# Performance work log

Measured on AMD Instinct MI355X. Metric: run time of the kernel, lower is better.

## Reference

```python
import jax, jax.numpy as jnp
import numpy as np

B, T, V, E, DH, H, M, W = 64, 50, 32000, 64, 128, 8, 256, 50


def setup_inputs() -> dict:
    key = jax.random.key(0)
    ks = jax.random.split(key, 18)
    sc = 0.02
    return {
        "x": jax.random.randint(ks[0], (B, T), 0, V),
        "tok_emb": jax.random.normal(ks[1], (V, E)) * sc,
        "pos_emb": jax.random.normal(ks[2], (W, E)) * sc,
        "Wq": jax.random.normal(ks[3], (H, E, DH)) * sc,
        "bq": jnp.zeros((H, DH)),
        "Wk": jax.random.normal(ks[4], (H, E, DH)) * sc,
        "bk": jnp.zeros((H, DH)),
        "Wv": jax.random.normal(ks[5], (H, E, DH)) * sc,
        "bv": jnp.zeros((H, DH)),
        "Wo": jax.random.normal(ks[6], (H * DH, E)) * sc,
        "bo": jnp.zeros((E,)),
        "W1": jax.random.normal(ks[7], (E, M)) * sc,
        "b1": jnp.zeros((M,)),
        "W2": jax.random.normal(ks[8], (M, E)) * sc,
        "b2": jnp.zeros((E,)),
        "Wf": jax.random.normal(ks[9], (E, V)) * sc,
        "bf": jnp.zeros((V,)),
    }


def reference(x, tok_emb, pos_emb, Wq, bq, Wk, bk, Wv, bv, Wo, bo, W1, b1, W2, b2, Wf, bf):
    b, t = x.shape
    h = tok_emb[x] + pos_emb[:t]  # [B,T,E]
    # batched per-head QKV projections (original loops over 8 heads)
    Q = jnp.einsum("bte,hed->bhtd", h, Wq) + bq[None, :, None, :]
    K = jnp.einsum("bte,hed->bhtd", h, Wk) + bk[None, :, None, :]
    Vv = jnp.einsum("bte,hed->bhtd", h, Wv) + bv[None, :, None, :]
    scores = jnp.einsum("bhtd,bhsd->bhts", Q, K) / (DH ** 0.5)
    # faithful to original: masked_fill(tril(scores) == 0, -inf)
    scores = jnp.where(jnp.tril(scores) == 0, -jnp.inf, scores)
    attn = jax.nn.softmax(scores, axis=-1)
    o = jnp.einsum("bhts,bhsd->bhtd", attn, Vv)
    o = o.transpose(0, 2, 1, 3).reshape(b, t, H * DH)  # concat heads
    a = o @ Wo + bo
    # NOTE: no residual connections in the original module
    m = jax.nn.gelu(a @ W1 + b1, approximate=False)
    y = m @ W2 + b2
    logits = y @ Wf + bf  # [B,T,V]
    return logits
```

## Files before the change

kernel.cpp:

```cpp
#include <hip/hip_runtime.h>
#include <math.h>

#define T_ 50
#define R_ 3200

using u16 = unsigned short;
typedef __attribute__((ext_vector_type(8))) __bf16 bf16x8;
typedef __attribute__((ext_vector_type(4))) float f32x4;

__device__ __forceinline__ float bf2f(u16 u) {
  union { unsigned int i; float f; } x; x.i = ((unsigned int)u) << 16; return x.f;
}
__device__ __forceinline__ u16 f2bf(float f) {
  union { float f; unsigned int i; } x; x.f = f;
  unsigned int r = x.i + 0x7FFFu + ((x.i >> 16) & 1u);
  return (u16)(r >> 16);
}
__device__ __forceinline__ void split2(float v, u16& hi, u16& lo) {
  hi = f2bf(v);
  lo = f2bf(v - bf2f(hi));
}
__device__ __forceinline__ float gelu_f(float v) {
  return 0.5f * v * (1.0f + erff(v * 0.70710678118654752f));
}

__global__ __launch_bounds__(256) void k_prep(
    const int* __restrict__ x, const float* __restrict__ tok, const float* __restrict__ pos,
    const float* __restrict__ Wq, const float* __restrict__ Wk, const float* __restrict__ Wv,
    const float* __restrict__ bq, const float* __restrict__ bk, const float* __restrict__ bv,
    const float* __restrict__ Wo, const float* __restrict__ W1, const float* __restrict__ W2,
    const float* __restrict__ Wf,
    u16* __restrict__ hH, u16* __restrict__ hL,
    u16* __restrict__ WqkvTh, u16* __restrict__ WqkvTl, float* __restrict__ bqkv,
    u16* __restrict__ WoTh, u16* __restrict__ WoTl,
    u16* __restrict__ W1Th, u16* __restrict__ W1Tl,
    u16* __restrict__ W2Th, u16* __restrict__ W2Tl,
    u16* __restrict__ WfTh, u16* __restrict__ WfTl) {
  __shared__ __align__(16) float tile[64][68];
  int bid = blockIdx.x;
  if (bid < 800) {
    int i = bid * 256 + threadIdx.x;
    int row = i >> 6, e = i & 63;
    int t = row % T_;
    int v = x[row];
    split2(tok[(long)v * 64 + e] + pos[t * 64 + e], hH[i], hL[i]);
    return;
  }
  if (bid < 1964) {
    int i = (bid - 800) * 256 + threadIdx.x;
    const int S0 = 196608, S1 = 3072, S2 = 65536, S3 = 16384;
    if (i < S0) {
      int n = i >> 6, e = i & 63;
      int p = n >> 10, rem = n & 1023;
      int hh_ = rem >> 7, d = rem & 127;
      const float* W = (p == 0) ? Wq : ((p == 1) ? Wk : Wv);
      split2(W[hh_ * 8192 + e * 128 + d], WqkvTh[i], WqkvTl[i]);
      return;
    }
    i -= S0;
    if (i < S1) { int p = i >> 10, rem = i & 1023;
      const float* bb = (p == 0) ? bq : ((p == 1) ? bk : bv);
      bqkv[i] = bb[rem]; return; }
    i -= S1;
    if (i < S2) { int n = i >> 10, k = i & 1023;
      split2(Wo[k * 64 + n], WoTh[i], WoTl[i]); return; }
    i -= S2;
    if (i < S3) { int n = i >> 6, k = i & 63;
      split2(W1[k * 256 + n], W1Th[i], W1Tl[i]); return; }
    i -= S3;
    { int n = i >> 8, k = i & 255;
      split2(W2[k * 64 + n], W2Th[i], W2Tl[i]); }
    return;
  }
  int n0 = (bid - 1964) * 64;
  for (int c = threadIdx.x; c < 1024; c += 256) {
    int k = c >> 4, ch = (c & 15) * 4;
    *(float4*)&tile[k][ch] = *(const float4*)&Wf[(long)k * 32000 + n0 + ch];
  }
  __syncthreads();
  for (int c = threadIdx.x; c < 1024; c += 256) {
    int n = c >> 4, ch = (c & 15) * 4;
    u16 th[4], tl[4];
#pragma unroll
    for (int j = 0; j < 4; ++j) split2(tile[ch + j][n], th[j], tl[j]);
    *(ushort4*)&WfTh[(long)(n0 + n) * 64 + ch] = *(ushort4*)th;
    *(ushort4*)&WfTl[(long)(n0 + n) * 64 + ch] = *(ushort4*)tl;
  }
}

__global__ __launch_bounds__(256) void k_attn(const float* __restrict__ QKV,
                                              u16* __restrict__ Oh,
                                              u16* __restrict__ Ol) {
  int bh = blockIdx.x;
  int b = bh >> 3, hd = bh & 7;
  __shared__ __align__(16) float Kl[64][133];
  __shared__ __align__(16) float Vl[T_][128];
  __shared__ float Qw[4][128];
  __shared__ float Pw[4][64];
  const int tid = threadIdx.x, lane = tid & 63, wave = tid >> 6;
  const float* base = QKV + (long)b * T_ * 3072 + hd * 128;
  for (int c = tid; c < T_ * 32; c += 256) {
    int s = c >> 5, c4 = (c & 31) * 4;
    float4 kv = *(const float4*)&base[(long)s * 3072 + 1024 + c4];
    Kl[s][c4] = kv.x; Kl[s][c4 + 1] = kv.y; Kl[s][c4 + 2] = kv.z; Kl[s][c4 + 3] = kv.w;
    *(float4*)&Vl[s][c4] = *(const float4*)&base[(long)s * 3072 + 2048 + c4];
  }
  for (int c = tid; c < 14 * 32; c += 256) {
    int s = 50 + (c >> 5), c4 = (c & 31) * 4;
    Kl[s][c4] = 0.f; Kl[s][c4 + 1] = 0.f; Kl[s][c4 + 2] = 0.f; Kl[s][c4 + 3] = 0.f;
  }
  __syncthreads();
  const float scale = 0.0883883476483184406f;
  for (int r = wave; r < T_; r += 4) {
    Qw[wave][lane] = base[(long)r * 3072 + lane];
    Qw[wave][64 + lane] = base[(long)r * 3072 + 64 + lane];
    float p = 0.f;
#pragma unroll 8
    for (int d = 0; d < 128; ++d) p += Qw[wave][d] * Kl[lane][d];
    float sc = (lane <= r) ? p * scale : -INFINITY;
    float mx = sc;
    mx = fmaxf(mx, __shfl_xor(mx, 32)); mx = fmaxf(mx, __shfl_xor(mx, 16));
    mx = fmaxf(mx, __shfl_xor(mx, 8));  mx = fmaxf(mx, __shfl_xor(mx, 4));
    mx = fmaxf(mx, __shfl_xor(mx, 2));  mx = fmaxf(mx, __shfl_xor(mx, 1));
    float e = expf(sc - mx);
    float sum = e;
    sum += __shfl_xor(sum, 32); sum += __shfl_xor(sum, 16); sum += __shfl_xor(sum, 8);
    sum += __shfl_xor(sum, 4);  sum += __shfl_xor(sum, 2);  sum += __shfl_xor(sum, 1);
    Pw[wave][lane] = e / sum;
    float o0 = 0.f, o1 = 0.f;
#pragma unroll 4
    for (int s = 0; s <= r; ++s) {
      float pv = Pw[wave][s];
      o0 += pv * Vl[s][lane];
      o1 += pv * Vl[s][64 + lane];
    }
    long orow = ((long)b * T_ + r) * 1024 + hd * 128;
    u16 hi, lo;
    split2(o0, hi, lo); Oh[orow + lane] = hi;      Ol[orow + lane] = lo;
    split2(o1, hi, lo); Oh[orow + 64 + lane] = hi; Ol[orow + 64 + lane] = lo;
  }
}

template <int BN, int BK, int ACT, int OSPLIT>
__global__ __launch_bounds__(256) void k_gemm(
    const u16* __restrict__ Ah, const u16* __restrict__ Al,
    const u16* __restrict__ Bth, const u16* __restrict__ Btl,
    const float* __restrict__ bias,
    float* __restrict__ C, u16* __restrict__ Ch, u16* __restrict__ Cl,
    int ldc, int K) {
  constexpr int BM = 64;
  constexpr int TN = BN / 16;
  constexpr int BKW = BK / 8;
  __shared__ __align__(16) u16 Bh[BN][BK + 8];
  __shared__ __align__(16) u16 Bl[BN][BK + 8];
  const int m0 = blockIdx.x * BM, n0 = blockIdx.y * BN;
  const int tid = threadIdx.x, lane = tid & 63, wave = tid >> 6;
  const int ln = lane & 15, quad = lane >> 4;
  const long arow = (long)(m0 + wave * 16 + ln) * K;
  f32x4 acc[TN];
#pragma unroll
  for (int tn = 0; tn < TN; ++tn)
#pragma unroll
    for (int i = 0; i < 4; ++i) acc[tn][i] = 0.f;

  for (int kk = 0; kk < K; kk += BK) {
#pragma unroll
    for (int c0 = 0; c0 < BN * BKW; c0 += 256) {
      int c = c0 + tid;
      int r = c / BKW, c8 = (c % BKW) * 8;
      *(uint4*)&Bh[r][c8] = *(const uint4*)&Bth[(long)(n0 + r) * K + kk + c8];
      *(uint4*)&Bl[r][c8] = *(const uint4*)&Btl[(long)(n0 + r) * K + kk + c8];
    }
    __syncthreads();
#pragma unroll
    for (int ks = 0; ks < BK / 32; ++ks) {
      bf16x8 a_h = *(const bf16x8*)&Ah[arow + kk + ks * 32 + quad * 8];
      bf16x8 a_l = *(const bf16x8*)&Al[arow + kk + ks * 32 + quad * 8];
#pragma unroll
      for (int tn = 0; tn < TN; ++tn) {
        bf16x8 b_h = *(const bf16x8*)&Bh[tn * 16 + ln][ks * 32 + quad * 8];
        bf16x8 b_l = *(const bf16x8*)&Bl[tn * 16 + ln][ks * 32 + quad * 8];
        acc[tn] = __builtin_amdgcn_mfma_f32_16x16x32_bf16(a_h, b_h, acc[tn], 0, 0, 0);
        acc[tn] = __builtin_amdgcn_mfma_f32_16x16x32_bf16(a_l, b_h, acc[tn], 0, 0, 0);
        acc[tn] = __builtin_amdgcn_mfma_f32_16x16x32_bf16(a_h, b_l, acc[tn], 0, 0, 0);
      }
    }
    __syncthreads();
  }
#pragma unroll
  for (int tn = 0; tn < TN; ++tn) {
    int col = n0 + tn * 16 + ln;
    float bv = bias[col];
#pragma unroll
    for (int rr = 0; rr < 4; ++rr) {
      float v = acc[tn][rr] + bv;
      if (ACT) v = gelu_f(v);
      long idx = (long)(m0 + wave * 16 + quad * 4 + rr) * ldc + col;
      if constexpr (OSPLIT) {
        u16 hi, lo; split2(v, hi, lo);
        Ch[idx] = hi; Cl[idx] = lo;
      } else {
        C[idx] = v;
      }
    }
  }
}

extern "C" void kernel_launch(void* const* d_in, const int* in_sizes, int n_in,
                              void* d_out, int out_size, void* d_ws, size_t ws_size,
                              hipStream_t stream) {
  const int*   x   = (const int*)d_in[0];
  const float* tok = (const float*)d_in[1];
  const float* pos = (const float*)d_in[2];
  const float* Wq  = (const float*)d_in[3];
  const float* bq  = (const float*)d_in[4];
  const float* Wk  = (const float*)d_in[5];
  const float* bk  = (const float*)d_in[6];
  const float* Wv  = (const float*)d_in[7];
  const float* bv  = (const float*)d_in[8];
  const float* Wo  = (const float*)d_in[9];
  const float* bo  = (const float*)d_in[10];
  const float* W1  = (const float*)d_in[11];
  const float* b1  = (const float*)d_in[12];
  const float* W2  = (const float*)d_in[13];
  const float* b2  = (const float*)d_in[14];
  const float* Wf  = (const float*)d_in[15];
  const float* bfv = (const float*)d_in[16];

  char* ws = (char*)d_ws;
  u16*   hH     = (u16*)(ws + 0);
  u16*   hL     = (u16*)(ws + 409600);
  float* QKV    = (float*)(ws + 819200);
  u16*   oH     = (u16*)(ws + 40140800);
  u16*   oL     = (u16*)(ws + 46694400);
  u16*   aH     = (u16*)(ws + 53248000);
  u16*   aL     = (u16*)(ws + 53657600);
  u16*   mH     = (u16*)(ws + 54067200);
  u16*   mL     = (u16*)(ws + 55705600);
  u16*   yH     = (u16*)(ws + 57344000);
  u16*   yL     = (u16*)(ws + 57753600);
  u16*   WqkvTh = (u16*)(ws + 58163200);
  u16*   WqkvTl = (u16*)(ws + 58556416);
  float* bqkv   = (float*)(ws + 58949632);
  u16*   WoTh   = (u16*)(ws + 58961920);
  u16*   WoTl   = (u16*)(ws + 59092992);
  u16*   W1Th   = (u16*)(ws + 59224064);
  u16*   W1Tl   = (u16*)(ws + 59256832);
  u16*   W2Th   = (u16*)(ws + 59289600);
  u16*   W2Tl   = (u16*)(ws + 59322368);
  u16*   WfTh   = (u16*)(ws + 59355136);
  u16*   WfTl   = (u16*)(ws + 63451136);
  float* out    = (float*)d_out;

  k_prep<<<dim3(2464), 256, 0, stream>>>(x, tok, pos, Wq, Wk, Wv, bq, bk, bv,
      Wo, W1, W2, Wf, hH, hL, WqkvTh, WqkvTl, bqkv, WoTh, WoTl,
      W1Th, W1Tl, W2Th, W2Tl, WfTh, WfTl);
  k_gemm<128, 64, 0, 0><<<dim3(50, 24), 256, 0, stream>>>(
      hH, hL, WqkvTh, WqkvTl, bqkv, QKV, nullptr, nullptr, 3072, 64);
  k_attn<<<dim3(512), 256, 0, stream>>>(QKV, oH, oL);
  k_gemm<64, 256, 0, 1><<<dim3(50, 1), 256, 0, stream>>>(
      oH, oL, WoTh, WoTl, bo, nullptr, aH, aL, 64, 1024);
  k_gemm<128, 64, 1, 1><<<dim3(50, 2), 256, 0, stream>>>(
      aH, aL, W1Th, W1Tl, b1, nullptr, mH, mL, 256, 64);
  k_gemm<64, 256, 0, 1><<<dim3(50, 1), 256, 0, stream>>>(
      mH, mL, W2Th, W2Tl, b2, nullptr, yH, yL, 64, 256);
  k_gemm<128, 64, 0, 0><<<dim3(50, 250), 256, 0, stream>>>(
      yH, yL, WfTh, WfTl, bfv, out, nullptr, nullptr, 32000, 64);
}
```

Baseline: 602.8 us.

## Fuse MLP chain, restructure attention, drop LDS staging in GEMM, add XCD swizzle

Merges the output-projection, W1+GELU and W2 GEMMs into one k_mlp kernel that keeps intermediates in shared memory, removing two launches and global round-trips. The attention kernel now processes four query rows per wave, with XOR-swizzled K and transposed V in LDS and vectorized loads. The generic GEMM reads B fragments straight from global memory instead of staging them in LDS, swaps the MFMA operands so the epilogue can write float4/ushort4 rows, and optionally remaps block IDs across XCDs for the large logits GEMM. The costs are more redundant global reads of B and a small 200-block MLP kernel with one wave per block, which may leave much of the device idle.

```diff
diff --git a/kernel.cpp b/kernel.cpp
--- a/kernel.cpp
+++ b/kernel.cpp
@@ -91,118 +91,262 @@
 __global__ __launch_bounds__(256) void k_attn(const float* __restrict__ QKV,
                                               u16* __restrict__ Oh,
                                               u16* __restrict__ Ol) {
-  int bh = blockIdx.x;
-  int b = bh >> 3, hd = bh & 7;
-  __shared__ __align__(16) float Kl[64][133];
-  __shared__ __align__(16) float Vl[T_][128];
-  __shared__ float Qw[4][128];
-  __shared__ float Pw[4][64];
+  __shared__ __align__(16) float Kl[64 * 128];
+  __shared__ __align__(16) float Vt[128 * 64];
+  __shared__ __align__(16) float Qw[4][512];
+  __shared__ __align__(16) float Pw[4][256];
+  const int bh = blockIdx.x, b = bh >> 3, hd = bh & 7;
   const int tid = threadIdx.x, lane = tid & 63, wave = tid >> 6;
   const float* base = QKV + (long)b * T_ * 3072 + hd * 128;
-  for (int c = tid; c < T_ * 32; c += 256) {
-    int s = c >> 5, c4 = (c & 31) * 4;
-    float4 kv = *(const float4*)&base[(long)s * 3072 + 1024 + c4];
-    Kl[s][c4] = kv.x; Kl[s][c4 + 1] = kv.y; Kl[s][c4 + 2] = kv.z; Kl[s][c4 + 3] = kv.w;
-    *(float4*)&Vl[s][c4] = *(const float4*)&base[(long)s * 3072 + 2048 + c4];
-  }
-  for (int c = tid; c < 14 * 32; c += 256) {
-    int s = 50 + (c >> 5), c4 = (c & 31) * 4;
-    Kl[s][c4] = 0.f; Kl[s][c4 + 1] = 0.f; Kl[s][c4 + 2] = 0.f; Kl[s][c4 + 3] = 0.f;
+  for (int c = tid; c < 64 * 32; c += 256) {
+    int s = c >> 5, c4 = c & 31;
+    float4 kv = make_float4(0.f, 0.f, 0.f, 0.f), vv = kv;
+    if (s < T_) {
+      const float* rowp = base + (long)s * 3072;
+      kv = *(const float4*)(rowp + 1024 + c4 * 4);
+      vv = *(const float4*)(rowp + 2048 + c4 * 4);
+    }
+    *(float4*)&Kl[s * 128 + ((c4 ^ (s & 31)) << 2)] = kv;
+    int d0 = c4 * 4, s4 = s >> 2, sm = s & 3;
+    Vt[(d0 + 0) * 64 + ((s4 ^ ((d0 + 0) & 15)) << 2) + sm] = vv.x;
+    Vt[(d0 + 1) * 64 + ((s4 ^ ((d0 + 1) & 15)) << 2) + sm] = vv.y;
+    Vt[(d0 + 2) * 64 + ((s4 ^ ((d0 + 2) & 15)) << 2) + sm] = vv.z;
+    Vt[(d0 + 3) * 64 + ((s4 ^ ((d0 + 3) & 15)) << 2) + sm] = vv.w;
   }
   __syncthreads();
   const float scale = 0.0883883476483184406f;
-  for (int r = wave; r < T_; r += 4) {
-    Qw[wave][lane] = base[(long)r * 3072 + lane];
-    Qw[wave][64 + lane] = base[(long)r * 3072 + 64 + lane];
-    float p = 0.f;
+  for (int g = wave; g < 13; g += 4) {
+    const int r0 = g * 4;
+#pragma unroll
+    for (int it = 0; it < 2; ++it) {
+      int cc = lane + it * 64;
+      int j = cc >> 5, c4q = cc & 31;
+      int rq = r0 + j;
+      if (rq < T_)
+        *(float4*)&Qw[wave][j * 128 + c4q * 4] =
+            *(const float4*)&base[(long)rq * 3072 + c4q * 4];
+    }
+    asm volatile("s_waitcnt lgkmcnt(0)" ::: "memory");
+    float p0 = 0.f, p1 = 0.f, p2 = 0.f, p3 = 0.f;
 #pragma unroll 8
-    for (int d = 0; d < 128; ++d) p += Qw[wave][d] * Kl[lane][d];
-    float sc = (lane <= r) ? p * scale : -INFINITY;
-    float mx = sc;
-    mx = fmaxf(mx, __shfl_xor(mx, 32)); mx = fmaxf(mx, __shfl_xor(mx, 16));
-    mx = fmaxf(mx, __shfl_xor(mx, 8));  mx = fmaxf(mx, __shfl_xor(mx, 4));
-    mx = fmaxf(mx, __shfl_xor(mx, 2));  mx = fmaxf(mx, __shfl_xor(mx, 1));
-    float e = expf(sc - mx);
-    float sum = e;
-    sum += __shfl_xor(sum, 32); sum += __shfl_xor(sum, 16); sum += __shfl_xor(sum, 8);
-    sum += __shfl_xor(sum, 4);  sum += __shfl_xor(sum, 2);  sum += __shfl_xor(sum, 1);
-    Pw[wave][lane] = e / sum;
-    float o0 = 0.f, o1 = 0.f;
-#pragma unroll 4
-    for (int s = 0; s <= r; ++s) {
-      float pv = Pw[wave][s];
-      o0 += pv * Vl[s][lane];
-      o1 += pv * Vl[s][64 + lane];
-    }
-    long orow = ((long)b * T_ + r) * 1024 + hd * 128;
-    u16 hi, lo;
-    split2(o0, hi, lo); Oh[orow + lane] = hi;      Ol[orow + lane] = lo;
-    split2(o1, hi, lo); Oh[orow + 64 + lane] = hi; Ol[orow + 64 + lane] = lo;
-  }
-}
-
-template <int BN, int BK, int ACT, int OSPLIT>
-__global__ __launch_bounds__(256) void k_gemm(
+    for (int c4 = 0; c4 < 32; ++c4) {
+      float4 kv = *(const float4*)&Kl[lane * 128 + ((c4 ^ (lane & 31)) << 2)];
+      float4 q0 = *(const float4*)&Qw[wave][c4 * 4];
+      float4 q1 = *(const float4*)&Qw[wave][128 + c4 * 4];
+      float4 q2 = *(const float4*)&Qw[wave][256 + c4 * 4];
+      float4 q3 = *(const float4*)&Qw[wave][384 + c4 * 4];
+      p0 = fmaf(q0.x, kv.x, p0); p0 = fmaf(q0.y, kv.y, p0);
+      p0 = fmaf(q0.z, kv.z, p0); p0 = fmaf(q0.w, kv.w, p0);
+      p1 = fmaf(q1.x, kv.x, p1); p1 = fmaf(q1.y, kv.y, p1);
+      p1 = fmaf(q1.z, kv.z, p1); p1 = fmaf(q1.w, kv.w, p1);
+      p2 = fmaf(q2.x, kv.x, p2); p2 = fmaf(q2.y, kv.y, p2);
+      p2 = fmaf(q2.z, kv.z, p2); p2 = fmaf(q2.w, kv.w, p2);
+      p3 = fmaf(q3.x, kv.x, p3); p3 = fmaf(q3.y, kv.y, p3);
+      p3 = fmaf(q3.z, kv.z, p3); p3 = fmaf(q3.w, kv.w, p3);
+    }
+    float ps[4] = {p0, p1, p2, p3};
+#pragma unroll
+    for (int j = 0; j < 4; ++j) {
+      int rq = r0 + j;
+      float sc = (rq < T_ && lane <= rq) ? ps[j] * scale : -INFINITY;
+      float mx = sc;
+      mx = fmaxf(mx, __shfl_xor(mx, 32)); mx = fmaxf(mx, __shfl_xor(mx, 16));
+      mx = fmaxf(mx, __shfl_xor(mx, 8));  mx = fmaxf(mx, __shfl_xor(mx, 4));
+      mx = fmaxf(mx, __shfl_xor(mx, 2));  mx = fmaxf(mx, __shfl_xor(mx, 1));
+      float e = expf(sc - mx);
+      float sum = e;
+      sum += __shfl_xor(sum, 32); sum += __shfl_xor(sum, 16); sum += __shfl_xor(sum, 8);
+      sum += __shfl_xor(sum, 4);  sum += __shfl_xor(sum, 2);  sum += __shfl_xor(sum, 1);
+      Pw[wave][j * 64 + lane] = e / sum;
+    }
+    asm volatile("s_waitcnt lgkmcnt(0)" ::: "memory");
+    float oa[4] = {0.f, 0.f, 0.f, 0.f};
+    float ob[4] = {0.f, 0.f, 0.f, 0.f};
+    for (int s4 = 0; s4 <= g; ++s4) {
+      int vc = (s4 ^ (lane & 15)) << 2;
+      float4 va = *(const float4*)&Vt[lane * 64 + vc];
+      float4 vb = *(const float4*)&Vt[(64 + lane) * 64 + vc];
+#pragma unroll
+      for (int j = 0; j < 4; ++j) {
+        float4 pb = *(const float4*)&Pw[wave][j * 64 + s4 * 4];
+        oa[j] = fmaf(pb.x, va.x, oa[j]); oa[j] = fmaf(pb.y, va.y, oa[j]);
+        oa[j] = fmaf(pb.z, va.z, oa[j]); oa[j] = fmaf(pb.w, va.w, oa[j]);
+        ob[j] = fmaf(pb.x, vb.x, ob[j]); ob[j] = fmaf(pb.y, vb.y, ob[j]);
+        ob[j] = fmaf(pb.z, vb.z, ob[j]); ob[j] = fmaf(pb.w, vb.w, ob[j]);
+      }
+    }
+#pragma unroll
+    for (int j = 0; j < 4; ++j) {
+      int rq = r0 + j;
+      if (rq < T_) {
+        long orow = ((long)b * T_ + rq) * 1024 + hd * 128;
+        u16 hi, lo;
+        split2(oa[j], hi, lo); Oh[orow + lane] = hi;      Ol[orow + lane] = lo;
+        split2(ob[j], hi, lo); Oh[orow + 64 + lane] = hi; Ol[orow + 64 + lane] = lo;
+      }
+    }
+  }
+}
+
+template <int WM, int TN, int KK, int ACT, int OSPLIT, int SWZ>
+__global__ __launch_bounds__(WM * 64) void k_gemm(
     const u16* __restrict__ Ah, const u16* __restrict__ Al,
     const u16* __restrict__ Bth, const u16* __restrict__ Btl,
     const float* __restrict__ bias,
     float* __restrict__ C, u16* __restrict__ Ch, u16* __restrict__ Cl,
-    int ldc, int K) {
-  constexpr int BM = 64;
-  constexpr int TN = BN / 16;
-  constexpr int BKW = BK / 8;
-  __shared__ __align__(16) u16 Bh[BN][BK + 8];
-  __shared__ __align__(16) u16 Bl[BN][BK + 8];
-  const int m0 = blockIdx.x * BM, n0 = blockIdx.y * BN;
+    int ldc, int gm) {
+  int id = blockIdx.x;
+  if constexpr (SWZ) {
+    int nbk = gridDim.x;
+    int q = nbk >> 3, r = nbk & 7;
+    int xcd = id & 7, idx = id >> 3;
+    id = (xcd < r ? xcd * (q + 1) : r * (q + 1) + (xcd - r) * q) + idx;
+  }
+  const int mb = id % gm, nb = id / gm;
+  const int m0 = mb * (WM * 16), n0 = nb * (TN * 16);
   const int tid = threadIdx.x, lane = tid & 63, wave = tid >> 6;
   const int ln = lane & 15, quad = lane >> 4;
-  const long arow = (long)(m0 + wave * 16 + ln) * K;
+  const int mrow = m0 + wave * 16 + ln;
+  const long arow = (long)mrow * KK;
   f32x4 acc[TN];
 #pragma unroll
   for (int tn = 0; tn < TN; ++tn)
 #pragma unroll
     for (int i = 0; i < 4; ++i) acc[tn][i] = 0.f;
-
-  for (int kk = 0; kk < K; kk += BK) {
-#pragma unroll
-    for (int c0 = 0; c0 < BN * BKW; c0 += 256) {
-      int c = c0 + tid;
-      int r = c / BKW, c8 = (c % BKW) * 8;
-      *(uint4*)&Bh[r][c8] = *(const uint4*)&Bth[(long)(n0 + r) * K + kk + c8];
-      *(uint4*)&Bl[r][c8] = *(const uint4*)&Btl[(long)(n0 + r) * K + kk + c8];
-    }
-    __syncthreads();
-#pragma unroll
-    for (int ks = 0; ks < BK / 32; ++ks) {
-      bf16x8 a_h = *(const bf16x8*)&Ah[arow + kk + ks * 32 + quad * 8];
-      bf16x8 a_l = *(const bf16x8*)&Al[arow + kk + ks * 32 + quad * 8];
-#pragma unroll
-      for (int tn = 0; tn < TN; ++tn) {
-        bf16x8 b_h = *(const bf16x8*)&Bh[tn * 16 + ln][ks * 32 + quad * 8];
-        bf16x8 b_l = *(const bf16x8*)&Bl[tn * 16 + ln][ks * 32 + quad * 8];
-        acc[tn] = __builtin_amdgcn_mfma_f32_16x16x32_bf16(a_h, b_h, acc[tn], 0, 0, 0);
-        acc[tn] = __builtin_amdgcn_mfma_f32_16x16x32_bf16(a_l, b_h, acc[tn], 0, 0, 0);
-        acc[tn] = __builtin_amdgcn_mfma_f32_16x16x32_bf16(a_h, b_l, acc[tn], 0, 0, 0);
-      }
-    }
-    __syncthreads();
+#pragma unroll
+  for (int k0 = 0; k0 < KK; k0 += 32) {
+    bf16x8 a_h = *(const bf16x8*)&Ah[arow + k0 + quad * 8];
+    bf16x8 a_l = *(const bf16x8*)&Al[arow + k0 + quad * 8];
+#pragma unroll
+    for (int tn = 0; tn < TN; ++tn) {
+      const long brow = (long)(n0 + tn * 16 + ln) * KK + k0 + quad * 8;
+      bf16x8 b_h = *(const bf16x8*)&Bth[brow];
+      bf16x8 b_l = *(const bf16x8*)&Btl[brow];
+      acc[tn] = __builtin_amdgcn_mfma_f32_16x16x32_bf16(b_h, a_h, acc[tn], 0, 0, 0);
+      acc[tn] = __builtin_amdgcn_mfma_f32_16x16x32_bf16(b_h, a_l, acc[tn], 0, 0, 0);
+      acc[tn] = __builtin_amdgcn_mfma_f32_16x16x32_bf16(b_l, a_h, acc[tn], 0, 0, 0);
+    }
   }
 #pragma unroll
   for (int tn = 0; tn < TN; ++tn) {
-    int col = n0 + tn * 16 + ln;
-    float bv = bias[col];
-#pragma unroll
-    for (int rr = 0; rr < 4; ++rr) {
-      float v = acc[tn][rr] + bv;
-      if (ACT) v = gelu_f(v);
-      long idx = (long)(m0 + wave * 16 + quad * 4 + rr) * ldc + col;
-      if constexpr (OSPLIT) {
-        u16 hi, lo; split2(v, hi, lo);
-        Ch[idx] = hi; Cl[idx] = lo;
-      } else {
-        C[idx] = v;
-      }
-    }
+    int nc = n0 + tn * 16 + quad * 4;
+    float4 bv = *(const float4*)&bias[nc];
+    float v0 = acc[tn][0] + bv.x, v1 = acc[tn][1] + bv.y;
+    float v2 = acc[tn][2] + bv.z, v3 = acc[tn][3] + bv.w;
+    if (ACT) { v0 = gelu_f(v0); v1 = gelu_f(v1); v2 = gelu_f(v2); v3 = gelu_f(v3); }
+    long idx2 = (long)mrow * ldc + nc;
+    if constexpr (OSPLIT) {
+      ushort4 hs, ls;
+      split2(v0, hs.x, ls.x); split2(v1, hs.y, ls.y);
+      split2(v2, hs.z, ls.z); split2(v3, hs.w, ls.w);
+      *(ushort4*)&Ch[idx2] = hs;
+      *(ushort4*)&Cl[idx2] = ls;
+    } else {
+      *(float4*)&C[idx2] = make_float4(v0, v1, v2, v3);
+    }
+  }
+}
+
+__global__ __launch_bounds__(64) void k_mlp(
+    const u16* __restrict__ oH, const u16* __restrict__ oL,
+    const u16* __restrict__ WoTh, const u16* __restrict__ WoTl, const float* __restrict__ bo,
+    const u16* __restrict__ W1Th, const u16* __restrict__ W1Tl, const float* __restrict__ b1,
+    const u16* __restrict__ W2Th, const u16* __restrict__ W2Tl, const float* __restrict__ b2,
+    u16* __restrict__ yH, u16* __restrict__ yL) {
+  __shared__ __align__(16) u16 aLh[16][88], aLl[16][88];
+  __shared__ __align__(16) u16 mLh[16][264], mLl[16][264];
+  const int lane = threadIdx.x, ln = lane & 15, quad = lane >> 4;
+  const int r = blockIdx.x * 16 + ln;
+  f32x4 acc1[4];
+#pragma unroll
+  for (int tn = 0; tn < 4; ++tn)
+#pragma unroll
+    for (int i = 0; i < 4; ++i) acc1[tn][i] = 0.f;
+#pragma unroll 4
+  for (int k0 = 0; k0 < 1024; k0 += 32) {
+    bf16x8 a_h = *(const bf16x8*)&oH[(long)r * 1024 + k0 + quad * 8];
+    bf16x8 a_l = *(const bf16x8*)&oL[(long)r * 1024 + k0 + quad * 8];
+#pragma unroll
+    for (int tn = 0; tn < 4; ++tn) {
+      const int brow = (tn * 16 + ln) * 1024 + k0 + quad * 8;
+      bf16x8 b_h = *(const bf16x8*)&WoTh[brow];
+      bf16x8 b_l = *(const bf16x8*)&WoTl[brow];
+      acc1[tn] = __builtin_amdgcn_mfma_f32_16x16x32_bf16(b_h, a_h, acc1[tn], 0, 0, 0);
+      acc1[tn] = __builtin_amdgcn_mfma_f32_16x16x32_bf16(b_h, a_l, acc1[tn], 0, 0, 0);
+      acc1[tn] = __builtin_amdgcn_mfma_f32_16x16x32_bf16(b_l, a_h, acc1[tn], 0, 0, 0);
+    }
+  }
+#pragma unroll
+  for (int tn = 0; tn < 4; ++tn) {
+    int nc = tn * 16 + quad * 4;
+    float4 bv = *(const float4*)&bo[nc];
+    ushort4 hs, ls;
+    split2(acc1[tn][0] + bv.x, hs.x, ls.x); split2(acc1[tn][1] + bv.y, hs.y, ls.y);
+    split2(acc1[tn][2] + bv.z, hs.z, ls.z); split2(acc1[tn][3] + bv.w, hs.w, ls.w);
+    *(ushort4*)&aLh[ln][nc] = hs;
+    *(ushort4*)&aLl[ln][nc] = ls;
+  }
+  __syncthreads();
+  f32x4 acc2[16];
+#pragma unroll
+  for (int tn = 0; tn < 16; ++tn)
+#pragma unroll
+    for (int i = 0; i < 4; ++i) acc2[tn][i] = 0.f;
+#pragma unroll
+  for (int k0 = 0; k0 < 64; k0 += 32) {
+    bf16x8 a_h = *(const bf16x8*)&aLh[ln][k0 + quad * 8];
+    bf16x8 a_l = *(const bf16x8*)&aLl[ln][k0 + quad * 8];
+#pragma unroll
+    for (int tn = 0; tn < 16; ++tn) {
+      const int brow = (tn * 16 + ln) * 64 + k0 + quad * 8;
+      bf16x8 b_h = *(const bf16x8*)&W1Th[brow];
+      bf16x8 b_l = *(const bf16x8*)&W1Tl[brow];
+      acc2[tn] = __builtin_amdgcn_mfma_f32_16x16x32_bf16(b_h, a_h, acc2[tn], 0, 0, 0);
+      acc2[tn] = __builtin_amdgcn_mfma_f32_16x16x32_bf16(b_h, a_l, acc2[tn], 0, 0, 0);
+      acc2[tn] = __builtin_amdgcn_mfma_f32_16x16x32_bf16(b_l, a_h, acc2[tn], 0, 0, 0);
+    }
+  }
+#pragma unroll
+  for (int tn = 0; tn < 16; ++tn) {
+    int nc = tn * 16 + quad * 4;
+    float4 bv = *(const float4*)&b1[nc];
+    ushort4 hs, ls;
+    split2(gelu_f(acc2[tn][0] + bv.x), hs.x, ls.x);
+    split2(gelu_f(acc2[tn][1] + bv.y), hs.y, ls.y);
+    split2(gelu_f(acc2[tn][2] + bv.z), hs.z, ls.z);
+    split2(gelu_f(acc2[tn][3] + bv.w), hs.w, ls.w);
+    *(ushort4*)&mLh[ln][nc] = hs;
+    *(ushort4*)&mLl[ln][nc] = ls;
+  }
+  __syncthreads();
+  f32x4 acc3[4];
+#pragma unroll
+  for (int tn = 0; tn < 4; ++tn)
+#pragma unroll
+    for (int i = 0; i < 4; ++i) acc3[tn][i] = 0.f;
+#pragma unroll 2
+  for (int k0 = 0; k0 < 256; k0 += 32) {
+    bf16x8 a_h = *(const bf16x8*)&mLh[ln][k0 + quad * 8];
+    bf16x8 a_l = *(const bf16x8*)&mLl[ln][k0 + quad * 8];
+#pragma unroll
+    for (int tn = 0; tn < 4; ++tn) {
+      const int brow = (tn * 16 + ln) * 256 + k0 + quad * 8;
+      bf16x8 b_h = *(const bf16x8*)&W2Th[brow];
+      bf16x8 b_l = *(const bf16x8*)&W2Tl[brow];
+      acc3[tn] = __builtin_amdgcn_mfma_f32_16x16x32_bf16(b_h, a_h, acc3[tn], 0, 0, 0);
+      acc3[tn] = __builtin_amdgcn_mfma_f32_16x16x32_bf16(b_h, a_l, acc3[tn], 0, 0, 0);
+      acc3[tn] = __builtin_amdgcn_mfma_f32_16x16x32_bf16(b_l, a_h, acc3[tn], 0, 0, 0);
+    }
+  }
+#pragma unroll
+  for (int tn = 0; tn < 4; ++tn) {
+    int nc = tn * 16 + quad * 4;
+    float4 bv = *(const float4*)&b2[nc];
+    ushort4 hs, ls;
+    split2(acc3[tn][0] + bv.x, hs.x, ls.x); split2(acc3[tn][1] + bv.y, hs.y, ls.y);
+    split2(acc3[tn][2] + bv.z, hs.z, ls.z); split2(acc3[tn][3] + bv.w, hs.w, ls.w);
+    *(ushort4*)&yH[(long)r * 64 + nc] = hs;
+    *(ushort4*)&yL[(long)r * 64 + nc] = ls;
   }
 }
 
@@ -228,42 +372,34 @@
   const float* bfv = (const float*)d_in[16];
 
   char* ws = (char*)d_ws;
-  u16*   hH     = (u16*)(ws + 0);
-  u16*   hL     = (u16*)(ws + 409600);
-  float* QKV    = (float*)(ws + 819200);
-  u16*   oH     = (u16*)(ws + 40140800);
-  u16*   oL     = (u16*)(ws + 46694400);
-  u16*   aH     = (u16*)(ws + 53248000);
-  u16*   aL     = (u16*)(ws + 53657600);
-  u16*   mH     = (u16*)(ws + 54067200);
-  u16*   mL     = (u16*)(ws + 55705600);
-  u16*   yH     = (u16*)(ws + 57344000);
-  u16*   yL     = (u16*)(ws + 57753600);
-  u16*   WqkvTh = (u16*)(ws + 58163200);
-  u16*   WqkvTl = (u16*)(ws + 58556416);
-  float* bqkv   = (float*)(ws + 58949632);
-  u16*   WoTh   = (u16*)(ws + 58961920);
-  u16*   WoTl   = (u16*)(ws + 59092992);
-  u16*   W1Th   = (u16*)(ws + 59224064);
-  u16*   W1Tl   = (u16*)(ws + 59256832);
-  u16*   W2Th   = (u16*)(ws + 59289600);
-  u16*   W2Tl   = (u16*)(ws + 59322368);
-  u16*   WfTh   = (u16*)(ws + 59355136);
-  u16*   WfTl   = (u16*)(ws + 63451136);
+  float* QKV    = (float*)(ws + 0);
+  u16*   oH     = (u16*)(ws + 39321600);
+  u16*   oL     = (u16*)(ws + 45875200);
+  u16*   hH     = (u16*)(ws + 52428800);
+  u16*   hL     = (u16*)(ws + 52838400);
+  u16*   yH     = (u16*)(ws + 53248000);
+  u16*   yL     = (u16*)(ws + 53657600);
+  u16*   WqkvTh = (u16*)(ws + 54067200);
+  u16*   WqkvTl = (u16*)(ws + 54460416);
+  float* bqkv   = (float*)(ws + 54853632);
+  u16*   WoTh   = (u16*)(ws + 54865920);
+  u16*   WoTl   = (u16*)(ws + 54996992);
+  u16*   W1Th   = (u16*)(ws + 55128064);
+  u16*   W1Tl   = (u16*)(ws + 55160832);
+  u16*   W2Th   = (u16*)(ws + 55193600);
+  u16*   W2Tl   = (u16*)(ws + 55226368);
+  u16*   WfTh   = (u16*)(ws + 55259136);
+  u16*   WfTl   = (u16*)(ws + 59355136);
   float* out    = (float*)d_out;
 
   k_prep<<<dim3(2464), 256, 0, stream>>>(x, tok, pos, Wq, Wk, Wv, bq, bk, bv,
       Wo, W1, W2, Wf, hH, hL, WqkvTh, WqkvTl, bqkv, WoTh, WoTl,
       W1Th, W1Tl, W2Th, W2Tl, WfTh, WfTl);
-  k_gemm<128, 64, 0, 0><<<dim3(50, 24), 256, 0, stream>>>(
-      hH, hL, WqkvTh, WqkvTl, bqkv, QKV, nullptr, nullptr, 3072, 64);
+  k_gemm<4, 8, 64, 0, 0, 0><<<dim3(1200), 256, 0, stream>>>(
+      hH, hL, WqkvTh, WqkvTl, bqkv, QKV, nullptr, nullptr, 3072, 50);
   k_attn<<<dim3(512), 256, 0, stream>>>(QKV, oH, oL);
-  k_gemm<64, 256, 0, 1><<<dim3(50, 1), 256, 0, stream>>>(
-      oH, oL, WoTh, WoTl, bo, nullptr, aH, aL, 64, 1024);
-  k_gemm<128, 64, 1, 1><<<dim3(50, 2), 256, 0, stream>>>(
-      aH, aL, W1Th, W1Tl, b1, nullptr, mH, mL, 256, 64);
-  k_gemm<64, 256, 0, 1><<<dim3(50, 1), 256, 0, stream>>>(
-      mH, mL, W2Th, W2Tl, b2, nullptr, yH, yL, 64, 256);
-  k_gemm<128, 64, 0, 0><<<dim3(50, 250), 256, 0, stream>>>(
-      yH, yL, WfTh, WfTl, bfv, out, nullptr, nullptr, 32000, 64);
-}
+  k_mlp<<<dim3(200), 64, 0, stream>>>(oH, oL, WoTh, WoTl, bo,
+      W1Th, W1Tl, b1, W2Th, W2Tl, b2, yH, yL);
+  k_gemm<4, 8, 64, 0, 0, 1><<<dim3(12500), 256, 0, stream>>>(
+      yH, yL, WfTh, WfTl, bfv, out, nullptr, nullptr, 32000, 50);
+}
```

New measurement: 732.9 us. 1.22x slower.
